# Kernel optimization log

Measured on AMD Instinct MI355X. Metric: run time of the kernel, lower is better.

## Reference

```python
import jax, jax.numpy as jnp
import numpy as np

B, SQ, SK, D, H, DH = 4, 1024, 1024, 1024, 16, 64

def setup_inputs() -> dict:
    key = jax.random.key(0)
    ks = jax.random.split(key, 7)
    s = 0.02
    return {
        "input_ids": jax.random.normal(ks[0], (B, SQ, D), jnp.float32),
        "encoder_output": jax.random.normal(ks[1], (B, SK, D), jnp.float32),
        "position_bias": jax.random.normal(ks[2], (1, H, SQ, SK), jnp.float32),
        "Wq": jax.random.normal(ks[3], (D, H * DH), jnp.float32) * s,
        "Wk": jax.random.normal(ks[4], (D, H * DH), jnp.float32) * s,
        "Wv": jax.random.normal(ks[5], (D, H * DH), jnp.float32) * s,
        "Wo": jax.random.normal(ks[6], (H * DH, D), jnp.float32) * s,
    }

def reference(input_ids, encoder_output, position_bias, Wq, Wk, Wv, Wo):
    # bias-free projections (nn.Linear(..., bias=False))
    q = (input_ids @ Wq).reshape(B, SQ, H, DH).transpose(0, 2, 1, 3)      # [B,H,Sq,dh]
    k = (encoder_output @ Wk).reshape(B, SK, H, DH).transpose(0, 2, 1, 3)  # [B,H,Sk,dh]
    v = (encoder_output @ Wv).reshape(B, SK, H, DH).transpose(0, 2, 1, 3)  # [B,H,Sk,dh]
    # T5-style attention: NO 1/sqrt(dh) scaling, additive position bias
    scores = jnp.einsum("bhqd,bhkd->bhqk", q, k) + position_bias          # [B,H,Sq,Sk]
    attn = jax.nn.softmax(scores, axis=-1)
    ctx = jnp.einsum("bhqk,bhkd->bhqd", attn, v)                          # [B,H,Sq,dh]
    ctx = ctx.transpose(0, 2, 1, 3).reshape(B, SQ, H * DH)
    return ctx @ Wo                                                        # [B,Sq,D]
```

## Files before the change

### kernel.cpp

```cpp
#include <hip/hip_runtime.h>

typedef _Float16 f16;
typedef _Float16 f16x4 __attribute__((ext_vector_type(4)));
typedef _Float16 f16x8 __attribute__((ext_vector_type(8)));
typedef float f32x4 __attribute__((ext_vector_type(4)));

#define LOADLDS16(gp, lp)                                                     \
  __builtin_amdgcn_global_load_lds(                                           \
      (const __attribute__((address_space(1))) void*)(gp),                    \
      (__attribute__((address_space(3))) void*)(lp), 16, 0, 0)

__global__ __launch_bounds__(256) void k_cast2(const float* __restrict__ a,
                                               const float* __restrict__ b,
                                               f16* __restrict__ ya,
                                               f16* __restrict__ yb) {
  int i = blockIdx.x * 256 + threadIdx.x;
  const float* x;
  f16* y;
  if (i < 1048576) {
    x = a; y = ya;
  } else {
    x = b; y = yb; i -= 1048576;
  }
  float4 v = reinterpret_cast<const float4*>(x)[i];
  f16x4 o;
  o[0] = (f16)v.x; o[1] = (f16)v.y; o[2] = (f16)v.z; o[3] = (f16)v.w;
  reinterpret_cast<f16x4*>(y)[i] = o;
}

__global__ __launch_bounds__(256) void k_castw_t(
    const float* __restrict__ w0, const float* __restrict__ w1,
    const float* __restrict__ w2, const float* __restrict__ w3,
    f16* __restrict__ o0, f16* __restrict__ o1, f16* __restrict__ o2,
    f16* __restrict__ o3) {
  const float* W;
  f16* O;
  switch (blockIdx.z) {
    case 0: W = w0; O = o0; break;
    case 1: W = w1; O = o1; break;
    case 2: W = w2; O = o2; break;
    default: W = w3; O = o3; break;
  }
  __shared__ f16 T[64][72];
  const int tid = threadIdx.x;
  const int r0 = blockIdx.y * 64, c0 = blockIdx.x * 64;
#pragma unroll
  for (int i = 0; i < 4; ++i) {
    int c = i * 256 + tid;
    int row = c >> 4, col = (c & 15) * 4;
    float4 v = *reinterpret_cast<const float4*>(W + (size_t)(r0 + row) * 1024 + c0 + col);
    T[col + 0][row] = (f16)v.x;
    T[col + 1][row] = (f16)v.y;
    T[col + 2][row] = (f16)v.z;
    T[col + 3][row] = (f16)v.w;
  }
  __syncthreads();
#pragma unroll
  for (int i = 0; i < 2; ++i) {
    int c = i * 256 + tid;
    int cc = c >> 3, ro = (c & 7) * 8;
    f16x8 v;
#pragma unroll
    for (int j = 0; j < 8; ++j) v[j] = T[cc][ro + j];
    *reinterpret_cast<f16x8*>(O + (size_t)(c0 + cc) * 1024 + r0 + ro) = v;
  }
}

__global__ __launch_bounds__(256) void k_gemm_qkv(const f16* __restrict__ Xq,
                                                  const f16* __restrict__ Xkv,
                                                  const f16* __restrict__ Bt,
                                                  f16* __restrict__ outp) {
  __shared__ f16 As[128 * 64];
  __shared__ f16 Bs[128 * 64];
  const int tid = threadIdx.x;
  const int w = tid >> 6, l = tid & 63;
  const int lr = l & 15, lq = l >> 4;
  const int m0 = blockIdx.y * 128, n0 = blockIdx.x * 128;
  const f16* A = (n0 < 1024) ? Xq : Xkv;
  const int wr = (w >> 1) * 64, wc = (w & 1) * 64;
  const int K = 1024;
  f32x4 acc[4][4] = {};
  for (int kt = 0; kt < K; kt += 64) {
#pragma unroll
    for (int i = 0; i < 4; ++i) {
      int c = (i * 4 + w) * 64 + l;
      LOADLDS16(A + (size_t)(m0 + (c >> 3)) * K + kt + (c & 7) * 8,
                As + (size_t)(i * 4 + w) * 512);
      LOADLDS16(Bt + (size_t)(n0 + (c >> 3)) * K + kt + (c & 7) * 8,
                Bs + (size_t)(i * 4 + w) * 512);
    }
    __syncthreads();
#pragma unroll
    for (int kk = 0; kk < 2; ++kk) {
      f16x8 af[4], bf[4];
#pragma unroll
      for (int m = 0; m < 4; ++m)
        af[m] = *reinterpret_cast<const f16x8*>(As + (wr + m * 16 + lr) * 64 + kk * 32 + lq * 8);
#pragma unroll
      for (int n = 0; n < 4; ++n)
        bf[n] = *reinterpret_cast<const f16x8*>(Bs + (wc + n * 16 + lr) * 64 + kk * 32 + lq * 8);
#pragma unroll
      for (int m = 0; m < 4; ++m)
#pragma unroll
        for (int n = 0; n < 4; ++n)
          acc[m][n] = __builtin_amdgcn_mfma_f32_16x16x32_f16(af[m], bf[n], acc[m][n], 0, 0, 0);
    }
    __syncthreads();
  }
#pragma unroll
  for (int m = 0; m < 4; ++m)
#pragma unroll
    for (int n = 0; n < 4; ++n)
#pragma unroll
      for (int r = 0; r < 4; ++r) {
        int row = m0 + wr + m * 16 + lq * 4 + r;
        int col = n0 + wc + n * 16 + lr;
        int b = row >> 10, s = row & 1023;
        int plane = col >> 10, cc = col & 1023;
        int h = cc >> 6, dh = cc & 63;
        outp[(size_t)plane * 4194304 +
             (((size_t)(b * 16 + h)) * 1024 + s) * 64 + dh] = (f16)acc[m][n][r];
      }
}

__global__ __launch_bounds__(256) void k_gemm_o(const f16* __restrict__ A,
                                                const f16* __restrict__ Bt,
                                                float* __restrict__ out, int M,
                                                int N, int K) {
  __shared__ f16 As[64 * 64];
  __shared__ f16 Bs[128 * 64];
  const int tid = threadIdx.x;
  const int w = tid >> 6, l = tid & 63;
  const int lr = l & 15, lq = l >> 4;
  const int m0 = blockIdx.y * 64, n0 = blockIdx.x * 128;
  const int wr = (w >> 1) * 32, wc = (w & 1) * 64;
  f32x4 acc[2][4] = {};
  for (int kt = 0; kt < K; kt += 64) {
#pragma unroll
    for (int i = 0; i < 2; ++i) {
      int c = (i * 4 + w) * 64 + l;
      LOADLDS16(A + (size_t)(m0 + (c >> 3)) * K + kt + (c & 7) * 8,
                As + (size_t)(i * 4 + w) * 512);
    }
#pragma unroll
    for (int i = 0; i < 4; ++i) {
      int c = (i * 4 + w) * 64 + l;
      LOADLDS16(Bt + (size_t)(n0 + (c >> 3)) * K + kt + (c & 7) * 8,
                Bs + (size_t)(i * 4 + w) * 512);
    }
    __syncthreads();
#pragma unroll
    for (int kk = 0; kk < 2; ++kk) {
      f16x8 af[2], bf[4];
#pragma unroll
      for (int m = 0; m < 2; ++m)
        af[m] = *reinterpret_cast<const f16x8*>(As + (wr + m * 16 + lr) * 64 + kk * 32 + lq * 8);
#pragma unroll
      for (int n = 0; n < 4; ++n)
        bf[n] = *reinterpret_cast<const f16x8*>(Bs + (wc + n * 16 + lr) * 64 + kk * 32 + lq * 8);
#pragma unroll
      for (int m = 0; m < 2; ++m)
#pragma unroll
        for (int n = 0; n < 4; ++n)
          acc[m][n] = __builtin_amdgcn_mfma_f32_16x16x32_f16(af[m], bf[n], acc[m][n], 0, 0, 0);
    }
    __syncthreads();
  }
#pragma unroll
  for (int m = 0; m < 2; ++m)
#pragma unroll
    for (int n = 0; n < 4; ++n)
#pragma unroll
      for (int r = 0; r < 4; ++r) {
        int row = m0 + wr + m * 16 + lq * 4 + r;
        int col = n0 + wc + n * 16 + lr;
        out[(size_t)row * N + col] = acc[m][n][r];
      }
}

__global__ __launch_bounds__(256) void k_vtrans(const f16* __restrict__ vb,
                                                f16* __restrict__ vtb) {
  const int bh = blockIdx.y, s0 = blockIdx.x * 64;
  __shared__ f16 T[64][72];
  const int tid = threadIdx.x;
  const f16* src = vb + (size_t)bh * 1024 * 64;
#pragma unroll
  for (int i = 0; i < 2; ++i) {
    int c = i * 256 + tid;
    int row = c >> 3, co = (c & 7) * 8;
    f16x8 v = *reinterpret_cast<const f16x8*>(src + (size_t)(s0 + row) * 64 + co);
#pragma unroll
    for (int j = 0; j < 8; ++j) T[co + j][row] = v[j];
  }
  __syncthreads();
  f16* dst = vtb + (size_t)bh * 64 * 1024;
#pragma unroll
  for (int i = 0; i < 2; ++i) {
    int c = i * 256 + tid;
    int dh = c >> 3, so = (c & 7) * 8;
    f16x8 v;
#pragma unroll
    for (int j = 0; j < 8; ++j) v[j] = T[dh][so + j];
    *reinterpret_cast<f16x8*>(dst + (size_t)dh * 1024 + s0 + so) = v;
  }
}

__global__ __launch_bounds__(256, 2) void k_attn(const f16* __restrict__ qb,
                                                 const f16* __restrict__ kb,
                                                 const f16* __restrict__ vtb,
                                                 const float* __restrict__ bias,
                                                 f16* __restrict__ ctx) {
  const int bid = blockIdx.x;
  const int ord = (bid & 7) * 64 + (bid >> 3);
  const int h = ord >> 5, qt = (ord >> 2) & 7, b = ord & 3;
  const int bh = b * 16 + h;
  const int q0 = qt * 128;
  const int tid = threadIdx.x, w = tid >> 6, l = tid & 63;
  const int lr = l & 15, lq = l >> 4;

  __shared__ f16 Kb3[3][2048];
  __shared__ f16 Vb3[3][2048];
  __shared__ f16 Ps[4][1280];

  const f16* qp = qb + ((size_t)bh * 1024 + q0 + w * 32 + lr) * 64 + lq * 8;
  f16x8 qA0 = *reinterpret_cast<const f16x8*>(qp);
  f16x8 qA1 = *reinterpret_cast<const f16x8*>(qp + 32);
  f16x8 qB0 = *reinterpret_cast<const f16x8*>(qp + 1024);
  f16x8 qB1 = *reinterpret_cast<const f16x8*>(qp + 1056);

  f32x4 OA[4] = {}, OB[4] = {};
  float mA = -3.0e38f, mB = -3.0e38f, rsA = 0.f, rsB = 0.f;

  const f16* kbase = kb + (size_t)bh * 65536;
  const f16* vbase = vtb + (size_t)bh * 65536;
  const float* bq0 =
      bias + ((size_t)h * 1024 + q0 + w * 32 + lr) * 1024 + lq * 4;
  const float* bq1 = bq0 + 16 * 1024;

  const int krow = w * 8 + (l >> 3), kg = (l & 7) ^ (l >> 3);
  const int vrow = w * 16 + (l >> 2), vg = (l & 3) ^ ((l >> 3) & 3);

  auto stage_kv = [&](int t, int c3) {
    LOADLDS16(kbase + (size_t)(t * 32 + krow) * 64 + kg * 8, &Kb3[c3][w * 512]);
    LOADLDS16(vbase + (size_t)vrow * 1024 + t * 32 + vg * 8, &Vb3[c3][w * 512]);
  };

  stage_kv(0, 0);
  stage_kv(1, 1);
  f32x4 bcA[2][2], bcB[2][2];
#pragma unroll
  for (int c = 0; c < 2; ++c) {
    bcA[0][c] = *reinterpret_cast<const f32x4*>(bq0 + c * 16);
    bcA[1][c] = *reinterpret_cast<const f32x4*>(bq1 + c * 16);
  }

  auto body = [&](int t, f32x4 (&bc)[2][2], f32x4 (&bn)[2][2]) {
    if (t == 31) {
      asm volatile("s_waitcnt vmcnt(4)" ::: "memory");
    } else {
      asm volatile("s_waitcnt vmcnt(6)" ::: "memory");
    }
    __builtin_amdgcn_s_barrier();
    __builtin_amdgcn_sched_barrier(0);

    if (t + 1 < 32) {
      const float* b0 = bq0 + (t + 1) * 32;
      const float* b1 = bq1 + (t + 1) * 32;
#pragma unroll
      for (int c = 0; c < 2; ++c) {
        bn[0][c] = *reinterpret_cast<const f32x4*>(b0 + c * 16);
        bn[1][c] = *reinterpret_cast<const f32x4*>(b1 + c * 16);
      }
    }
    if (t + 2 < 32) stage_kv(t + 2, (t + 2) % 3);
    __builtin_amdgcn_sched_barrier(0);

    const int c3 = t % 3;
    const f16* Kc = &Kb3[c3][0];
    const f16* Vc = &Vb3[c3][0];

    f32x4 S[2][2] = {};
    __builtin_amdgcn_s_setprio(1);
#pragma unroll
    for (int c = 0; c < 2; ++c) {
      int row = c * 16 + lr;
      const f16* kbp = &Kc[row * 64];
      f16x8 kf0 = *reinterpret_cast<const f16x8*>(kbp + ((lq ^ (lr & 7)) * 8));
      f16x8 kf1 = *reinterpret_cast<const f16x8*>(kbp + (((4 + lq) ^ (lr & 7)) * 8));
      S[0][c] = __builtin_amdgcn_mfma_f32_16x16x32_f16(kf0, qA0, S[0][c], 0, 0, 0);
      S[0][c] = __builtin_amdgcn_mfma_f32_16x16x32_f16(kf1, qA1, S[0][c], 0, 0, 0);
      S[1][c] = __builtin_amdgcn_mfma_f32_16x16x32_f16(kf0, qB0, S[1][c], 0, 0, 0);
      S[1][c] = __builtin_amdgcn_mfma_f32_16x16x32_f16(kf1, qB1, S[1][c], 0, 0, 0);
    }
    __builtin_amdgcn_s_setprio(0);

#pragma unroll
    for (int f = 0; f < 2; ++f)
#pragma unroll
      for (int c = 0; c < 2; ++c)
#pragma unroll
        for (int r = 0; r < 4; ++r) S[f][c][r] += bc[f][c][r];

    float tA = fmaxf(fmaxf(fmaxf(S[0][0][0], S[0][0][1]), fmaxf(S[0][0][2], S[0][0][3])),
                     fmaxf(fmaxf(S[0][1][0], S[0][1][1]), fmaxf(S[0][1][2], S[0][1][3])));
    float tB = fmaxf(fmaxf(fmaxf(S[1][0][0], S[1][0][1]), fmaxf(S[1][0][2], S[1][0][3])),
                     fmaxf(fmaxf(S[1][1][0], S[1][1][1]), fmaxf(S[1][1][2], S[1][1][3])));
    bool ok = (tA <= mA + 8.0f) && (tB <= mB + 8.0f);
    if (!__all(ok)) {
      tA = fmaxf(tA, __shfl_xor(tA, 16, 64));
      tA = fmaxf(tA, __shfl_xor(tA, 32, 64));
      tB = fmaxf(tB, __shfl_xor(tB, 16, 64));
      tB = fmaxf(tB, __shfl_xor(tB, 32, 64));
      float mnA = fmaxf(mA, tA), mnB = fmaxf(mB, tB);
      float scA = __expf(mA - mnA), scB = __expf(mB - mnB);
      mA = mnA; mB = mnB;
      rsA *= scA; rsB *= scB;
      int sb = l & 48;
#pragma unroll
      for (int r = 0; r < 4; ++r) {
        float sA = __shfl(scA, sb | (lq * 4 + r), 64);
        float sB = __shfl(scB, sb | (lq * 4 + r), 64);
#pragma unroll
        for (int c = 0; c < 4; ++c) {
          OA[c][r] *= sA;
          OB[c][r] *= sB;
        }
      }
    }

#pragma unroll
    for (int c = 0; c < 2; ++c) {
      f32x4 pA, pB;
#pragma unroll
      for (int r = 0; r < 4; ++r) {
        pA[r] = __expf(S[0][c][r] - mA);
        pB[r] = __expf(S[1][c][r] - mB);
      }
      rsA += (pA[0] + pA[1]) + (pA[2] + pA[3]);
      rsB += (pB[0] + pB[1]) + (pB[2] + pB[3]);
      f16x4 hA = {(f16)pA[0], (f16)pA[1], (f16)pA[2], (f16)pA[3]};
      f16x4 hB = {(f16)pB[0], (f16)pB[1], (f16)pB[2], (f16)pB[3]};
      *reinterpret_cast<f16x4*>(&Ps[w][lr * 40 + c * 16 + lq * 4]) = hA;
      *reinterpret_cast<f16x4*>(&Ps[w][(16 + lr) * 40 + c * 16 + lq * 4]) = hB;
    }

    {
      f16x8 paA = *reinterpret_cast<const f16x8*>(&Ps[w][lr * 40 + lq * 8]);
      f16x8 paB = *reinterpret_cast<const f16x8*>(&Ps[w][(16 + lr) * 40 + lq * 8]);
      __builtin_amdgcn_s_setprio(1);
#pragma unroll
      for (int c = 0; c < 4; ++c) {
        int row = c * 16 + lr;
        f16x8 vf = *reinterpret_cast<const f16x8*>(
            &Vc[row * 32 + ((lq ^ ((lr >> 1) & 3)) * 8)]);
        OA[c] = __builtin_amdgcn_mfma_f32_16x16x32_f16(paA, vf, OA[c], 0, 0, 0);
        OB[c] = __builtin_amdgcn_mfma_f32_16x16x32_f16(paB, vf, OB[c], 0, 0, 0);
      }
      __builtin_amdgcn_s_setprio(0);
    }
  };

#pragma unroll 1
  for (int ith = 0; ith < 16; ++ith) {
    body(2 * ith, bcA, bcB);
    body(2 * ith + 1, bcB, bcA);
  }

  rsA += __shfl_xor(rsA, 16, 64);
  rsA += __shfl_xor(rsA, 32, 64);
  rsB += __shfl_xor(rsB, 16, 64);
  rsB += __shfl_xor(rsB, 32, 64);
  int sb = l & 48;

#pragma unroll
  for (int r = 0; r < 4; ++r) {
    float dA = __shfl(rsA, sb | (lq * 4 + r), 64);
    float dB = __shfl(rsB, sb | (lq * 4 + r), 64);
    int rowA = q0 + w * 32 + lq * 4 + r;
#pragma unroll
    for (int c = 0; c < 4; ++c) {
      int col = h * 64 + c * 16 + lr;
      ctx[((size_t)b * 1024 + rowA) * 1024 + col] = (f16)(OA[c][r] / dA);
      ctx[((size_t)b * 1024 + rowA + 16) * 1024 + col] = (f16)(OB[c][r] / dB);
    }
  }
}

extern "C" void kernel_launch(void* const* d_in, const int* in_sizes, int n_in,
                              void* d_out, int out_size, void* d_ws,
                              size_t ws_size, hipStream_t stream) {
  const float* input_ids = (const float*)d_in[0];
  const float* enc = (const float*)d_in[1];
  const float* bias = (const float*)d_in[2];
  const float* Wq = (const float*)d_in[3];
  const float* Wk = (const float*)d_in[4];
  const float* Wv = (const float*)d_in[5];
  const float* Wo = (const float*)d_in[6];

  char* ws = (char*)d_ws;
  const size_t MB = 1024 * 1024;
  f16* Xq  = (f16*)(ws + 0 * MB);
  f16* Xkv = (f16*)(ws + 8 * MB);
  f16* Wqt = (f16*)(ws + 16 * MB);
  f16* Wkt = (f16*)(ws + 18 * MB);
  f16* Wvt = (f16*)(ws + 20 * MB);
  f16* Wot = (f16*)(ws + 22 * MB);
  f16* qbuf = (f16*)(ws + 24 * MB);
  f16* kbuf = (f16*)(ws + 32 * MB);
  f16* vbuf = (f16*)(ws + 40 * MB);
  f16* vtb = Xkv;
  f16* ctxb = Xq;

  k_cast2<<<8192, 256, 0, stream>>>(input_ids, enc, Xq, Xkv);
  k_castw_t<<<dim3(16, 16, 4), 256, 0, stream>>>(Wq, Wk, Wv, Wo, Wqt, Wkt, Wvt, Wot);

  k_gemm_qkv<<<dim3(24, 32), 256, 0, stream>>>(Xq, Xkv, Wqt, qbuf);

  k_vtrans<<<dim3(16, 64), 256, 0, stream>>>(vbuf, vtb);

  k_attn<<<512, 256, 0, stream>>>(qbuf, kbuf, vtb, bias, ctxb);

  k_gemm_o<<<dim3(8, 64), 256, 0, stream>>>(ctxb, Wot, (float*)d_out, 4096, 1024, 1024);
}
```

Measured before the change: 141.8 us.

## Load K/V fragments directly from global memory instead of LDS triple-buffering

Removes the LDS triple-buffered K/V staging via global_load_lds, along with its waitcnt/barrier pipeline and the double-buffered bias prefetch. Each wave now loads its K, V and bias fragments straight from global memory into registers every iteration, and the launch-bounds occupancy hint is dropped. This cuts LDS traffic and block-wide barriers, but every wave now fetches K/V itself, relying on L2/L1 for reuse, and there is no software prefetch to hide global-load latency.

After: 184.1 us. +29.9%, slower.

```diff
diff --git a/kernel.cpp b/kernel.cpp
--- a/kernel.cpp
+++ b/kernel.cpp
@@ -205,11 +205,11 @@
   }
 }
 
-__global__ __launch_bounds__(256, 2) void k_attn(const f16* __restrict__ qb,
-                                                 const f16* __restrict__ kb,
-                                                 const f16* __restrict__ vtb,
-                                                 const float* __restrict__ bias,
-                                                 f16* __restrict__ ctx) {
+__global__ __launch_bounds__(256) void k_attn(const f16* __restrict__ qb,
+                                              const f16* __restrict__ kb,
+                                              const f16* __restrict__ vtb,
+                                              const float* __restrict__ bias,
+                                              f16* __restrict__ ctx) {
   const int bid = blockIdx.x;
   const int ord = (bid & 7) * 64 + (bid >> 3);
   const int h = ord >> 5, qt = (ord >> 2) & 7, b = ord & 3;
@@ -218,8 +218,6 @@
   const int tid = threadIdx.x, w = tid >> 6, l = tid & 63;
   const int lr = l & 15, lq = l >> 4;
 
-  __shared__ f16 Kb3[3][2048];
-  __shared__ f16 Vb3[3][2048];
   __shared__ f16 Ps[4][1280];
 
   const f16* qp = qb + ((size_t)bh * 1024 + q0 + w * 32 + lr) * 64 + lq * 8;
@@ -231,66 +229,40 @@
   f32x4 OA[4] = {}, OB[4] = {};
   float mA = -3.0e38f, mB = -3.0e38f, rsA = 0.f, rsB = 0.f;
 
-  const f16* kbase = kb + (size_t)bh * 65536;
-  const f16* vbase = vtb + (size_t)bh * 65536;
+  const f16* kp0 = kb + (size_t)bh * 65536 + (size_t)lr * 64 + lq * 8;
+  const f16* vp0 = vtb + (size_t)bh * 65536 + (size_t)lr * 1024 + lq * 8;
   const float* bq0 =
       bias + ((size_t)h * 1024 + q0 + w * 32 + lr) * 1024 + lq * 4;
   const float* bq1 = bq0 + 16 * 1024;
 
-  const int krow = w * 8 + (l >> 3), kg = (l & 7) ^ (l >> 3);
-  const int vrow = w * 16 + (l >> 2), vg = (l & 3) ^ ((l >> 3) & 3);
-
-  auto stage_kv = [&](int t, int c3) {
-    LOADLDS16(kbase + (size_t)(t * 32 + krow) * 64 + kg * 8, &Kb3[c3][w * 512]);
-    LOADLDS16(vbase + (size_t)vrow * 1024 + t * 32 + vg * 8, &Vb3[c3][w * 512]);
-  };
-
-  stage_kv(0, 0);
-  stage_kv(1, 1);
-  f32x4 bcA[2][2], bcB[2][2];
-#pragma unroll
-  for (int c = 0; c < 2; ++c) {
-    bcA[0][c] = *reinterpret_cast<const f32x4*>(bq0 + c * 16);
-    bcA[1][c] = *reinterpret_cast<const f32x4*>(bq1 + c * 16);
-  }
-
-  auto body = [&](int t, f32x4 (&bc)[2][2], f32x4 (&bn)[2][2]) {
-    if (t == 31) {
-      asm volatile("s_waitcnt vmcnt(4)" ::: "memory");
-    } else {
-      asm volatile("s_waitcnt vmcnt(6)" ::: "memory");
-    }
-    __builtin_amdgcn_s_barrier();
-    __builtin_amdgcn_sched_barrier(0);
-
-    if (t + 1 < 32) {
-      const float* b0 = bq0 + (t + 1) * 32;
-      const float* b1 = bq1 + (t + 1) * 32;
-#pragma unroll
-      for (int c = 0; c < 2; ++c) {
-        bn[0][c] = *reinterpret_cast<const f32x4*>(b0 + c * 16);
-        bn[1][c] = *reinterpret_cast<const f32x4*>(b1 + c * 16);
-      }
-    }
-    if (t + 2 < 32) stage_kv(t + 2, (t + 2) % 3);
-    __builtin_amdgcn_sched_barrier(0);
-
-    const int c3 = t % 3;
-    const f16* Kc = &Kb3[c3][0];
-    const f16* Vc = &Vb3[c3][0];
+#pragma unroll 1
+  for (int t = 0; t < 32; ++t) {
+    f16x8 kf[2][2];
+#pragma unroll
+    for (int c = 0; c < 2; ++c) {
+      const f16* kp = kp0 + (size_t)(t * 32 + c * 16) * 64;
+      kf[c][0] = *reinterpret_cast<const f16x8*>(kp);
+      kf[c][1] = *reinterpret_cast<const f16x8*>(kp + 32);
+    }
+    f32x4 bf[2][2];
+#pragma unroll
+    for (int c = 0; c < 2; ++c) {
+      bf[0][c] = *reinterpret_cast<const f32x4*>(bq0 + t * 32 + c * 16);
+      bf[1][c] = *reinterpret_cast<const f32x4*>(bq1 + t * 32 + c * 16);
+    }
+    f16x8 vf[4];
+#pragma unroll
+    for (int c = 0; c < 4; ++c)
+      vf[c] = *reinterpret_cast<const f16x8*>(vp0 + (size_t)c * 16 * 1024 + t * 32);
 
     f32x4 S[2][2] = {};
     __builtin_amdgcn_s_setprio(1);
 #pragma unroll
     for (int c = 0; c < 2; ++c) {
-      int row = c * 16 + lr;
-      const f16* kbp = &Kc[row * 64];
-      f16x8 kf0 = *reinterpret_cast<const f16x8*>(kbp + ((lq ^ (lr & 7)) * 8));
-      f16x8 kf1 = *reinterpret_cast<const f16x8*>(kbp + (((4 + lq) ^ (lr & 7)) * 8));
-      S[0][c] = __builtin_amdgcn_mfma_f32_16x16x32_f16(kf0, qA0, S[0][c], 0, 0, 0);
-      S[0][c] = __builtin_amdgcn_mfma_f32_16x16x32_f16(kf1, qA1, S[0][c], 0, 0, 0);
-      S[1][c] = __builtin_amdgcn_mfma_f32_16x16x32_f16(kf0, qB0, S[1][c], 0, 0, 0);
-      S[1][c] = __builtin_amdgcn_mfma_f32_16x16x32_f16(kf1, qB1, S[1][c], 0, 0, 0);
+      S[0][c] = __builtin_amdgcn_mfma_f32_16x16x32_f16(kf[c][0], qA0, S[0][c], 0, 0, 0);
+      S[0][c] = __builtin_amdgcn_mfma_f32_16x16x32_f16(kf[c][1], qA1, S[0][c], 0, 0, 0);
+      S[1][c] = __builtin_amdgcn_mfma_f32_16x16x32_f16(kf[c][0], qB0, S[1][c], 0, 0, 0);
+      S[1][c] = __builtin_amdgcn_mfma_f32_16x16x32_f16(kf[c][1], qB1, S[1][c], 0, 0, 0);
     }
     __builtin_amdgcn_s_setprio(0);
 
@@ -299,7 +271,7 @@
 #pragma unroll
       for (int c = 0; c < 2; ++c)
 #pragma unroll
-        for (int r = 0; r < 4; ++r) S[f][c][r] += bc[f][c][r];
+        for (int r = 0; r < 4; ++r) S[f][c][r] += bf[f][c][r];
 
     float tA = fmaxf(fmaxf(fmaxf(S[0][0][0], S[0][0][1]), fmaxf(S[0][0][2], S[0][0][3])),
                      fmaxf(fmaxf(S[0][1][0], S[0][1][1]), fmaxf(S[0][1][2], S[0][1][3])));
@@ -350,20 +322,11 @@
       __builtin_amdgcn_s_setprio(1);
 #pragma unroll
       for (int c = 0; c < 4; ++c) {
-        int row = c * 16 + lr;
-        f16x8 vf = *reinterpret_cast<const f16x8*>(
-            &Vc[row * 32 + ((lq ^ ((lr >> 1) & 3)) * 8)]);
-        OA[c] = __builtin_amdgcn_mfma_f32_16x16x32_f16(paA, vf, OA[c], 0, 0, 0);
-        OB[c] = __builtin_amdgcn_mfma_f32_16x16x32_f16(paB, vf, OB[c], 0, 0, 0);
+        OA[c] = __builtin_amdgcn_mfma_f32_16x16x32_f16(paA, vf[c], OA[c], 0, 0, 0);
+        OB[c] = __builtin_amdgcn_mfma_f32_16x16x32_f16(paB, vf[c], OB[c], 0, 0, 0);
       }
       __builtin_amdgcn_s_setprio(0);
     }
-  };
-
-#pragma unroll 1
-  for (int ith = 0; ith < 16; ++ith) {
-    body(2 * ith, bcA, bcB);
-    body(2 * ith + 1, bcB, bcA);
   }
 
   rsA += __shfl_xor(rsA, 16, 64);
```
